# Performance work log

Hardware: AMD Instinct MI355X
Metric: run time of the kernel (lower is better)

The kernel has to match this reference:

```python
import jax, jax.numpy as jnp
import numpy as np

TOKENS, D_IN, D_OUT = 8192, 4096, 11008


def setup_inputs() -> dict:
    key = jax.random.key(0)
    k1, k2, k3, k4 = jax.random.split(key, 4)
    x = jax.random.normal(k1, (TOKENS, D_IN), dtype=jnp.float32)
    # int8-range quantized weight (stored int32; values in [-127, 127] simulated via [0,127])
    weight_q = jax.random.randint(k2, (D_OUT, D_IN), -127, 128, dtype=jnp.int32)
    # per-output-row scale (abs-max / 127), small positive values
    max_val = jax.random.uniform(k3, (D_OUT,), dtype=jnp.float32, minval=1e-3, maxval=0.02)
    bias = jax.random.normal(k4, (D_OUT,), dtype=jnp.float32)
    return {"x": x, "weight_q": weight_q, "max_val": max_val, "bias": bias}


def reference(x, weight_q, max_val, bias):
    # dequantize: w[o, i] = weight_q[o, i] * max_val[o]   (per-row scale)
    w = weight_q.astype(x.dtype) * max_val[:, None]          # [D_OUT, D_IN]
    # linear: y = x @ w.T + bias
    return jnp.einsum('ti,oi->to', x, w) + bias               # [TOKENS, D_OUT]
```

## Files before the change

### kernel.cpp

```cpp
#include <hip/hip_runtime.h>


#define M_TOK 8192
#define K_DIM 4096
#define N_OUT 11008
#define BM 256
#define BN 256
#define BK 64
#define NT (K_DIM / BK)
#define NBM (M_TOK / BM)
#define NBN (N_OUT / BN)
#define NWG (NBM * NBN)
#define SLOT 32768

typedef __attribute__((ext_vector_type(4))) int   i32x4;
typedef __attribute__((ext_vector_type(4))) float f32x4;
typedef __attribute__((ext_vector_type(4))) short bf16x4;
typedef __attribute__((ext_vector_type(8))) short bf16x8;
typedef unsigned short u16;
typedef signed char i8;
typedef unsigned char u8;

__global__ __launch_bounds__(256) void prep_fused(
    const float* __restrict__ x, i8* __restrict__ xq, float* __restrict__ sx,
    const int* __restrict__ win, i8* __restrict__ wout, long n16) {
  __shared__ float wmx[4];
  const int tid = threadIdx.x;
  if (blockIdx.x < M_TOK) {
    const int t = blockIdx.x;
    const float* row = x + (long)t * K_DIM;
    f32x4 v[4];
    float mx = 0.0f;
#pragma unroll
    for (int j = 0; j < 4; ++j) {
      v[j] = ((const f32x4*)row)[tid * 4 + j];
#pragma unroll
      for (int e = 0; e < 4; ++e) mx = fmaxf(mx, fabsf(v[j][e]));
    }
#pragma unroll
    for (int off = 32; off >= 1; off >>= 1) mx = fmaxf(mx, __shfl_xor(mx, off));
    if ((tid & 63) == 0) wmx[tid >> 6] = mx;
    __syncthreads();
    mx = fmaxf(fmaxf(wmx[0], wmx[1]), fmaxf(wmx[2], wmx[3]));
    const float sxinv = (mx > 0.0f) ? 127.0f / mx : 0.0f;
    if (tid == 0) sx[t] = (mx > 0.0f) ? mx / 127.0f : 0.0f;
    i32x4 out;
#pragma unroll
    for (int j = 0; j < 4; ++j) {
      int q0 = __float2int_rn(v[j][0] * sxinv);
      int q1 = __float2int_rn(v[j][1] * sxinv);
      int q2 = __float2int_rn(v[j][2] * sxinv);
      int q3 = __float2int_rn(v[j][3] * sxinv);
      q0 = max(-127, min(127, q0)); q1 = max(-127, min(127, q1));
      q2 = max(-127, min(127, q2)); q3 = max(-127, min(127, q3));
      out[j] = (q0 & 255) | ((q1 & 255) << 8) | ((q2 & 255) << 16) | ((q3 & 255) << 24);
    }
    ((i32x4*)(xq + (long)t * K_DIM))[tid] = out;
  } else {
    long i = (long)(blockIdx.x - M_TOK) * blockDim.x + tid;
    const long stride = 2048L * blockDim.x;
    for (; i < n16; i += stride) {
      i32x4 o;
#pragma unroll
      for (int j = 0; j < 4; ++j) {
        i32x4 w = ((const i32x4*)win)[i * 4 + j];
        o[j] = (w[0] & 255) | ((w[1] & 255) << 8) | ((w[2] & 255) << 16) | ((w[3] & 255) << 24);
      }
      ((i32x4*)wout)[i] = o;
    }
  }
}

__device__ __forceinline__ void gl_lds16(const i8* g, u8* l) {
  __builtin_amdgcn_global_load_lds(
      (const __attribute__((address_space(1))) void*)g,
      (__attribute__((address_space(3))) void*)l,
      16, 0, 0);
}

#define STAGE(T) do { \
    u8* wp = lds + ((T) & 3) * SLOT; \
    const int ko_ = (T) * BK; \
    gl_lds16(pA + ko_, wp + dwa); \
    gl_lds16(pB + ko_, wp + 16384 + dwa); \
  } while (0)

#define TILE(T, ST, CNTASM) do { \
    const char* pa_ = ldsc + ((T) & 3) * SLOT + abase; \
    const char* pb_ = ldsc + ((T) & 3) * SLOT + bbase; \
    i32x4 af[4], bv[4]; \
    _Pragma("unroll") \
    for (int m = 0; m < 4; ++m) af[m] = *(const i32x4*)(pa_ + m * 1024); \
    _Pragma("unroll") \
    for (int n = 0; n < 4; ++n) bv[n] = *(const i32x4*)(pb_ + n * 1024); \
    if (ST) STAGE((T) + 3); \
    __builtin_amdgcn_s_setprio(1); \
    _Pragma("unroll") \
    for (int m = 0; m < 4; ++m) \
      _Pragma("unroll") \
      for (int n = 0; n < 4; ++n) \
        acc[m][n] = __builtin_amdgcn_mfma_i32_16x16x64_i8(af[m], bv[n], acc[m][n], 0, 0, 0); \
    __builtin_amdgcn_s_setprio(0); \
    asm volatile(CNTASM ::: "memory"); \
    __builtin_amdgcn_sched_barrier(0); \
    __builtin_amdgcn_s_barrier(); \
  } while (0)

__global__ __launch_bounds__(1024, 4) void gemm_i8(
    const i8* __restrict__ A, const i8* __restrict__ B,
    const float* __restrict__ sx, const float* __restrict__ scale,
    const float* __restrict__ bias, float* __restrict__ C) {
  __shared__ u8 lds[4 * SLOT];

  const int tid  = threadIdx.x;
  const int lane = tid & 63;
  const int wave = tid >> 6;
  const int wm = wave >> 2;
  const int wn = wave & 3;

  const int swz = (blockIdx.x & 7) * (NWG / 8) + (blockIdx.x >> 3);
  const int bm = swz / NBN;
  const int bn = swz % NBN;
  const long m0 = (long)bm * BM;
  const long n0 = (long)bn * BN;

  const int rs = tid >> 2;
  const int cs = ((tid & 3) * 16) ^ (((tid >> 3) & 3) << 4);
  const i8* pA = A + (m0 + rs) * (long)K_DIM + cs;
  const i8* pB = B + (n0 + rs) * (long)K_DIM + cs;
  const int dwa = wave * 1024;

  const int inner = ((lane >> 4) * 16) ^ ((((lane & 15) >> 1) & 3) << 4);
  const int abase = (wm * 64 + (lane & 15)) * 64 + inner;
  const int bbase = 16384 + (wn * 64 + (lane & 15)) * 64 + inner;
  const char* ldsc = (const char*)lds;

  i32x4 acc[4][4] = {};

  STAGE(0); STAGE(1); STAGE(2);
  asm volatile("s_waitcnt vmcnt(4)" ::: "memory");
  __builtin_amdgcn_sched_barrier(0);
  __builtin_amdgcn_s_barrier();

  for (int t = 0; t < NT - 3; ++t) {
    TILE(t, 1, "s_waitcnt vmcnt(4)");
  }
  TILE(NT - 3, 0, "s_waitcnt vmcnt(2)");
  TILE(NT - 2, 0, "s_waitcnt vmcnt(0)");
  TILE(NT - 1, 0, "s_waitcnt vmcnt(0)");

  const int crow = (lane >> 4) * 4;
  const int ccol = lane & 15;
  float sxa[4][4];
#pragma unroll
  for (int m = 0; m < 4; ++m)
#pragma unroll
    for (int v = 0; v < 4; ++v)
      sxa[m][v] = sx[m0 + wm * 64 + m * 16 + crow + v];
#pragma unroll
  for (int n = 0; n < 4; ++n) {
    const long col = n0 + wn * 64 + n * 16 + ccol;
    const float sc = scale[col];
    const float bz = bias[col];
#pragma unroll
    for (int m = 0; m < 4; ++m) {
      const long row = m0 + wm * 64 + m * 16 + crow;
      i32x4 a = acc[m][n];
#pragma unroll
      for (int v = 0; v < 4; ++v)
        C[(row + v) * (long)N_OUT + col] = (float)a[v] * (sc * sxa[m][v]) + bz;
    }
  }
}

__device__ __forceinline__ u16 to_bf16_rne(float f) {
  union { float f; unsigned u; } v; v.f = f;
  return (u16)((v.u + 0x7FFFu + ((v.u >> 16) & 1u)) >> 16);
}

__global__ __launch_bounds__(256) void gemm_cvt(
    const float* __restrict__ X, const int* __restrict__ W,
    const float* __restrict__ scale, const float* __restrict__ bias,
    float* __restrict__ C) {
  __shared__ u16 lds_a[128 * 32];
  __shared__ u16 lds_b[128 * 32];

  const int tid  = threadIdx.x;
  const int lane = tid & 63;
  const int wave = tid >> 6;
  const int wm = wave >> 1, wn = wave & 1;

  const long m0 = (long)blockIdx.y * 128;
  const long n0 = (long)blockIdx.x * 128;

  const int arow = tid >> 3;
  const int acol = (tid & 7) * 4;

  const float* gX = X + (m0 + arow) * (long)K_DIM + acol;
  const int*   gW = W + (n0 + arow) * (long)K_DIM + acol;

  u16* wla = lds_a + arow * 32 + acol;
  u16* wlb = lds_b + arow * 32 + acol;

  f32x4 acc[4][4] = {};
  const int fr = lane & 15;
  const int fk = (lane >> 4) * 8;
  const u16* fa = lds_a + (wm * 64 + fr) * 32 + fk;
  const u16* fb = lds_b + (wn * 64 + fr) * 32 + fk;

  for (int kk = 0; kk < K_DIM / 32; ++kk) {
    const long ko = (long)kk * 32;
    f32x4 xv[4]; i32x4 wv[4];
#pragma unroll
    for (int j = 0; j < 4; ++j) {
      xv[j] = *(const f32x4*)(gX + (long)j * 32 * K_DIM + ko);
      wv[j] = *(const i32x4*)(gW + (long)j * 32 * K_DIM + ko);
    }
    __syncthreads();
#pragma unroll
    for (int j = 0; j < 4; ++j) {
      bf16x4 oa, ob;
      oa.x = (short)to_bf16_rne(xv[j][0]);
      oa.y = (short)to_bf16_rne(xv[j][1]);
      oa.z = (short)to_bf16_rne(xv[j][2]);
      oa.w = (short)to_bf16_rne(xv[j][3]);
      ob.x = (short)to_bf16_rne((float)wv[j][0]);
      ob.y = (short)to_bf16_rne((float)wv[j][1]);
      ob.z = (short)to_bf16_rne((float)wv[j][2]);
      ob.w = (short)to_bf16_rne((float)wv[j][3]);
      *(bf16x4*)(wla + j * 32 * 32) = oa;
      *(bf16x4*)(wlb + j * 32 * 32) = ob;
    }
    __syncthreads();

    bf16x8 af[4], bfr[4];
#pragma unroll
    for (int m = 0; m < 4; ++m) af[m] = *(const bf16x8*)(fa + m * 16 * 32);
#pragma unroll
    for (int n = 0; n < 4; ++n) bfr[n] = *(const bf16x8*)(fb + n * 16 * 32);
#pragma unroll
    for (int m = 0; m < 4; ++m)
#pragma unroll
      for (int n = 0; n < 4; ++n)
        acc[m][n] = __builtin_amdgcn_mfma_f32_16x16x32_bf16(af[m], bfr[n], acc[m][n], 0, 0, 0);
  }

  const int crow = (lane >> 4) * 4;
  const int ccol = lane & 15;
#pragma unroll
  for (int n = 0; n < 4; ++n) {
    const long col = n0 + wn * 64 + n * 16 + ccol;
    const float sc = scale[col];
    const float bz = bias[col];
#pragma unroll
    for (int m = 0; m < 4; ++m) {
      const long row = m0 + wm * 64 + m * 16 + crow;
      f32x4 a = acc[m][n];
#pragma unroll
      for (int v = 0; v < 4; ++v)
        C[(row + v) * (long)N_OUT + col] = a[v] * sc + bz;
    }
  }
}

extern "C" void kernel_launch(void* const* d_in, const int* in_sizes, int n_in,
                              void* d_out, int out_size, void* d_ws, size_t ws_size,
                              hipStream_t stream) {
  const float* x  = (const float*)d_in[0];
  const int*   wq = (const int*)d_in[1];
  const float* mx = (const float*)d_in[2];
  const float* bs = (const float*)d_in[3];
  float* out = (float*)d_out;

  const size_t szXQ = (size_t)M_TOK * K_DIM;
  const size_t szWQ = (size_t)N_OUT * K_DIM;
  const size_t szSX = (size_t)M_TOK * sizeof(float);
  if (ws_size >= szXQ + szWQ + szSX) {
    i8* xq = (i8*)d_ws;
    i8* wq8 = xq + szXQ;
    float* sx = (float*)(wq8 + szWQ);
    prep_fused<<<M_TOK + 2048, 256, 0, stream>>>(x, xq, sx, wq, wq8,
                                                 (long)N_OUT * K_DIM / 16);
    gemm_i8<<<dim3(NWG), dim3(1024), 0, stream>>>(xq, wq8, sx, mx, bs, out);
  } else {
    dim3 grid(N_OUT / 128, M_TOK / 128);
    gemm_cvt<<<grid, 256, 0, stream>>>(x, wq, mx, bs, out);
  }
}
```

Measured before the change: 477.7 us.

## Double-buffer A fragments in registers and prefetch next tile from LDS

A-operand fragments for tile T+1 are now read from LDS during tile T into alternating register sets (afE/afO), so those LDS reads overlap the current tile's MFMAs. The main loop is unrolled by two to alternate the buffers. The MFMA loop order is swapped to n-outer. The vmcnt waits are tightened from 4 to 2 so the next stage's global-to-LDS loads have landed one tile earlier, which shortens the effective prefetch distance and adds register pressure.

```diff
diff --git a/kernel.cpp b/kernel.cpp
--- a/kernel.cpp
+++ b/kernel.cpp
@@ -85,21 +85,23 @@
     gl_lds16(pB + ko_, wp + 16384 + dwa); \
   } while (0)
 
-#define TILE(T, ST, CNTASM) do { \
-    const char* pa_ = ldsc + ((T) & 3) * SLOT + abase; \
+#define TILE(T, AFC, AFN, RA, ST, CNTASM) do { \
     const char* pb_ = ldsc + ((T) & 3) * SLOT + bbase; \
-    i32x4 af[4], bv[4]; \
-    _Pragma("unroll") \
-    for (int m = 0; m < 4; ++m) af[m] = *(const i32x4*)(pa_ + m * 1024); \
+    i32x4 bv[4]; \
     _Pragma("unroll") \
     for (int n = 0; n < 4; ++n) bv[n] = *(const i32x4*)(pb_ + n * 1024); \
+    if (RA) { \
+      const char* pa1_ = ldsc + (((T) + 1) & 3) * SLOT + abase; \
+      _Pragma("unroll") \
+      for (int m = 0; m < 4; ++m) AFN[m] = *(const i32x4*)(pa1_ + m * 1024); \
+    } \
     if (ST) STAGE((T) + 3); \
     __builtin_amdgcn_s_setprio(1); \
     _Pragma("unroll") \
-    for (int m = 0; m < 4; ++m) \
+    for (int n = 0; n < 4; ++n) \
       _Pragma("unroll") \
-      for (int n = 0; n < 4; ++n) \
-        acc[m][n] = __builtin_amdgcn_mfma_i32_16x16x64_i8(af[m], bv[n], acc[m][n], 0, 0, 0); \
+      for (int m = 0; m < 4; ++m) \
+        acc[m][n] = __builtin_amdgcn_mfma_i32_16x16x64_i8(AFC[m], bv[n], acc[m][n], 0, 0, 0); \
     __builtin_amdgcn_s_setprio(0); \
     asm volatile(CNTASM ::: "memory"); \
     __builtin_amdgcn_sched_barrier(0); \
@@ -136,18 +138,26 @@
   const char* ldsc = (const char*)lds;
 
   i32x4 acc[4][4] = {};
+  i32x4 afE[4], afO[4];
 
   STAGE(0); STAGE(1); STAGE(2);
-  asm volatile("s_waitcnt vmcnt(4)" ::: "memory");
+  asm volatile("s_waitcnt vmcnt(2)" ::: "memory");
   __builtin_amdgcn_sched_barrier(0);
   __builtin_amdgcn_s_barrier();
-
-  for (int t = 0; t < NT - 3; ++t) {
-    TILE(t, 1, "s_waitcnt vmcnt(4)");
-  }
-  TILE(NT - 3, 0, "s_waitcnt vmcnt(2)");
-  TILE(NT - 2, 0, "s_waitcnt vmcnt(0)");
-  TILE(NT - 1, 0, "s_waitcnt vmcnt(0)");
+  {
+    const char* qa = ldsc + abase;
+#pragma unroll
+    for (int m = 0; m < 4; ++m) afE[m] = *(const i32x4*)(qa + m * 1024);
+  }
+
+  for (int t = 0; t < 60; t += 2) {
+    TILE(t,     afE, afO, 1, 1, "s_waitcnt vmcnt(2)");
+    TILE(t + 1, afO, afE, 1, 1, "s_waitcnt vmcnt(2)");
+  }
+  TILE(60, afE, afO, 1, 1, "s_waitcnt vmcnt(2)");
+  TILE(61, afO, afE, 1, 0, "s_waitcnt vmcnt(0)");
+  TILE(62, afE, afO, 1, 0, "s_waitcnt vmcnt(0)");
+  TILE(63, afO, afE, 0, 0, "s_waitcnt vmcnt(0)");
 
   const int crow = (lane >> 4) * 4;
   const int ccol = lane & 15;
```

After: 511.3 us. +7.0%, slower.

## Restructure int8 GEMM to 512 threads, BK=128, double-buffered sub-tile pipeline

Applied to the files above, without the earlier changes.

Halves the workgroup to 8 waves, each now computing a 128x64 output block with 8x4 accumulators, and doubles BK to 128. Each K-tile is split into two 64-wide halves, and each half is computed in two phases. Global-to-LDS loads for the next tile are interleaved between these phases, replacing the previous 4-slot ring. The aim is more MFMA work per LDS fragment load, since B fragments are reused across 8 M sub-tiles, and better overlap of loads with compute. In exchange it roughly doubles accumulator registers, adds more barriers per tile, and uses 128KB of LDS, which may limit occupancy.

```diff
diff --git a/kernel.cpp b/kernel.cpp
--- a/kernel.cpp
+++ b/kernel.cpp
@@ -6,12 +6,11 @@
 #define N_OUT 11008
 #define BM 256
 #define BN 256
-#define BK 64
+#define BK 128
 #define NT (K_DIM / BK)
 #define NBM (M_TOK / BM)
 #define NBN (N_OUT / BN)
 #define NWG (NBM * NBN)
-#define SLOT 32768
 
 typedef __attribute__((ext_vector_type(4))) int   i32x4;
 typedef __attribute__((ext_vector_type(4))) float f32x4;
@@ -78,22 +77,37 @@
       16, 0, 0);
 }
 
-#define STAGE(T) do { \
-    u8* wp = lds + ((T) & 3) * SLOT; \
-    const int ko_ = (T) * BK; \
-    gl_lds16(pA + ko_, wp + dwa); \
-    gl_lds16(pB + ko_, wp + 16384 + dwa); \
+#define SA(KT, SUB) do { \
+    const int bo_ = (((KT) & 1) << 16) + ((SUB) << 14); \
+    const i8* s_ = pA0 + (KT) * BK + (SUB) * 64; \
+    gl_lds16(s_, lds + bo_ + dwa); \
+    gl_lds16(s_ + 128L * K_DIM, lds + bo_ + 8192 + dwa); \
   } while (0)
-
-#define TILE(T, ST, CNTASM) do { \
-    const char* pa_ = ldsc + ((T) & 3) * SLOT + abase; \
-    const char* pb_ = ldsc + ((T) & 3) * SLOT + bbase; \
+#define SB(KT, SUB) do { \
+    const int bo_ = (((KT) & 1) << 16) + 32768 + ((SUB) << 14); \
+    const i8* s_ = pB0 + (KT) * BK + (SUB) * 64; \
+    gl_lds16(s_, lds + bo_ + dwa); \
+    gl_lds16(s_ + 128L * K_DIM, lds + bo_ + 8192 + dwa); \
+  } while (0)
+
+#define BAR() __builtin_amdgcn_s_barrier()
+#define LGKM0() do { asm volatile("s_waitcnt lgkmcnt(0)" ::: "memory"); \
+                     __builtin_amdgcn_sched_barrier(0); } while (0)
+
+#define TILE(T, S12, S34, C2, C4) do { \
+    const char* base_ = ldsc + (((T) & 1) << 16); \
+    const char* pa0_ = base_ + abase;             \
+    const char* pa1_ = base_ + 16384 + abase;     \
+    const char* pb0_ = base_ + 32768 + bbase;     \
+    const char* pb1_ = base_ + 49152 + bbase;     \
     i32x4 af[4], bv[4]; \
-    _Pragma("unroll") \
-    for (int m = 0; m < 4; ++m) af[m] = *(const i32x4*)(pa_ + m * 1024); \
-    _Pragma("unroll") \
-    for (int n = 0; n < 4; ++n) bv[n] = *(const i32x4*)(pb_ + n * 1024); \
-    if (ST) STAGE((T) + 3); \
+     \
+    _Pragma("unroll") \
+    for (int m = 0; m < 4; ++m) af[m] = *(const i32x4*)(pa0_ + m * 1024); \
+    _Pragma("unroll") \
+    for (int n = 0; n < 4; ++n) bv[n] = *(const i32x4*)(pb0_ + n * 1024); \
+    if (S12) SA((T) + 1, 1); \
+    BAR(); LGKM0(); \
     __builtin_amdgcn_s_setprio(1); \
     _Pragma("unroll") \
     for (int m = 0; m < 4; ++m) \
@@ -101,16 +115,62 @@
       for (int n = 0; n < 4; ++n) \
         acc[m][n] = __builtin_amdgcn_mfma_i32_16x16x64_i8(af[m], bv[n], acc[m][n], 0, 0, 0); \
     __builtin_amdgcn_s_setprio(0); \
-    asm volatile(CNTASM ::: "memory"); \
+    BAR(); \
+     \
+    i32x4 ag[4]; \
+    _Pragma("unroll") \
+    for (int m = 0; m < 4; ++m) ag[m] = *(const i32x4*)(pa0_ + (m + 4) * 1024); \
+    if (S12) SB((T) + 1, 1); \
+    BAR(); LGKM0(); \
+    __builtin_amdgcn_s_setprio(1); \
+    _Pragma("unroll") \
+    for (int m = 0; m < 4; ++m) \
+      _Pragma("unroll") \
+      for (int n = 0; n < 4; ++n) \
+        acc[m + 4][n] = __builtin_amdgcn_mfma_i32_16x16x64_i8(ag[m], bv[n], acc[m + 4][n], 0, 0, 0); \
+    __builtin_amdgcn_s_setprio(0); \
+    asm volatile(C2 ::: "memory"); \
     __builtin_amdgcn_sched_barrier(0); \
-    __builtin_amdgcn_s_barrier(); \
+    BAR(); \
+     \
+    i32x4 af1[4], bw[4]; \
+    _Pragma("unroll") \
+    for (int m = 0; m < 4; ++m) af1[m] = *(const i32x4*)(pa1_ + m * 1024); \
+    _Pragma("unroll") \
+    for (int n = 0; n < 4; ++n) bw[n] = *(const i32x4*)(pb1_ + n * 1024); \
+    if (S34) SA((T) + 2, 0); \
+    BAR(); LGKM0(); \
+    __builtin_amdgcn_s_setprio(1); \
+    _Pragma("unroll") \
+    for (int m = 0; m < 4; ++m) \
+      _Pragma("unroll") \
+      for (int n = 0; n < 4; ++n) \
+        acc[m][n] = __builtin_amdgcn_mfma_i32_16x16x64_i8(af1[m], bw[n], acc[m][n], 0, 0, 0); \
+    __builtin_amdgcn_s_setprio(0); \
+    BAR(); \
+     \
+    i32x4 ag1[4]; \
+    _Pragma("unroll") \
+    for (int m = 0; m < 4; ++m) ag1[m] = *(const i32x4*)(pa1_ + (m + 4) * 1024); \
+    if (S34) SB((T) + 2, 0); \
+    BAR(); LGKM0(); \
+    __builtin_amdgcn_s_setprio(1); \
+    _Pragma("unroll") \
+    for (int m = 0; m < 4; ++m) \
+      _Pragma("unroll") \
+      for (int n = 0; n < 4; ++n) \
+        acc[m + 4][n] = __builtin_amdgcn_mfma_i32_16x16x64_i8(ag1[m], bw[n], acc[m + 4][n], 0, 0, 0); \
+    __builtin_amdgcn_s_setprio(0); \
+    asm volatile(C4 ::: "memory"); \
+    __builtin_amdgcn_sched_barrier(0); \
+    BAR(); \
   } while (0)
 
-__global__ __launch_bounds__(1024, 4) void gemm_i8(
+__global__ __launch_bounds__(512, 2) void gemm_i8(
     const i8* __restrict__ A, const i8* __restrict__ B,
     const float* __restrict__ sx, const float* __restrict__ scale,
     const float* __restrict__ bias, float* __restrict__ C) {
-  __shared__ u8 lds[4 * SLOT];
+  __shared__ u8 lds[131072];
 
   const int tid  = threadIdx.x;
   const int lane = tid & 63;
@@ -126,45 +186,44 @@
 
   const int rs = tid >> 2;
   const int cs = ((tid & 3) * 16) ^ (((tid >> 3) & 3) << 4);
-  const i8* pA = A + (m0 + rs) * (long)K_DIM + cs;
-  const i8* pB = B + (n0 + rs) * (long)K_DIM + cs;
+  const i8* pA0 = A + (m0 + rs) * (long)K_DIM + cs;
+  const i8* pB0 = B + (n0 + rs) * (long)K_DIM + cs;
   const int dwa = wave * 1024;
 
   const int inner = ((lane >> 4) * 16) ^ ((((lane & 15) >> 1) & 3) << 4);
-  const int abase = (wm * 64 + (lane & 15)) * 64 + inner;
-  const int bbase = 16384 + (wn * 64 + (lane & 15)) * 64 + inner;
+  const int abase = (wm * 128 + (lane & 15)) * 64 + inner;
+  const int bbase = (wn * 64 + (lane & 15)) * 64 + inner;
   const char* ldsc = (const char*)lds;
 
-  i32x4 acc[4][4] = {};
-
-  STAGE(0); STAGE(1); STAGE(2);
+  i32x4 acc[8][4] = {};
+
+  SA(0, 0); SB(0, 0); SA(0, 1); SB(0, 1); SA(1, 0); SB(1, 0);
   asm volatile("s_waitcnt vmcnt(4)" ::: "memory");
   __builtin_amdgcn_sched_barrier(0);
-  __builtin_amdgcn_s_barrier();
-
-  for (int t = 0; t < NT - 3; ++t) {
-    TILE(t, 1, "s_waitcnt vmcnt(4)");
-  }
-  TILE(NT - 3, 0, "s_waitcnt vmcnt(2)");
-  TILE(NT - 2, 0, "s_waitcnt vmcnt(0)");
-  TILE(NT - 1, 0, "s_waitcnt vmcnt(0)");
+  BAR();
+
+  for (int t = 0; t < NT - 2; ++t) {
+    TILE(t, 1, 1, "s_waitcnt vmcnt(4)", "s_waitcnt vmcnt(4)");
+  }
+  TILE(NT - 2, 1, 0, "s_waitcnt vmcnt(4)", "s_waitcnt vmcnt(4)");
+  TILE(NT - 1, 0, 0, "s_waitcnt vmcnt(0)", "s_waitcnt vmcnt(0)");
 
   const int crow = (lane >> 4) * 4;
   const int ccol = lane & 15;
-  float sxa[4][4];
-#pragma unroll
-  for (int m = 0; m < 4; ++m)
+  float sxa[8][4];
+#pragma unroll
+  for (int m = 0; m < 8; ++m)
 #pragma unroll
     for (int v = 0; v < 4; ++v)
-      sxa[m][v] = sx[m0 + wm * 64 + m * 16 + crow + v];
+      sxa[m][v] = sx[m0 + wm * 128 + m * 16 + crow + v];
 #pragma unroll
   for (int n = 0; n < 4; ++n) {
     const long col = n0 + wn * 64 + n * 16 + ccol;
     const float sc = scale[col];
     const float bz = bias[col];
 #pragma unroll
-    for (int m = 0; m < 4; ++m) {
-      const long row = m0 + wm * 64 + m * 16 + crow;
+    for (int m = 0; m < 8; ++m) {
+      const long row = m0 + wm * 128 + m * 16 + crow;
       i32x4 a = acc[m][n];
 #pragma unroll
       for (int v = 0; v < 4; ++v)
@@ -281,7 +340,7 @@
     float* sx = (float*)(wq8 + szWQ);
     prep_fused<<<M_TOK + 2048, 256, 0, stream>>>(x, xq, sx, wq, wq8,
                                                  (long)N_OUT * K_DIM / 16);
-    gemm_i8<<<dim3(NWG), dim3(1024), 0, stream>>>(xq, wq8, sx, mx, bs, out);
+    gemm_i8<<<dim3(NWG), dim3(512), 0, stream>>>(xq, wq8, sx, mx, bs, out);
   } else {
     dim3 grid(N_OUT / 128, M_TOK / 128);
     gemm_cvt<<<grid, 256, 0, stream>>>(x, wq, mx, bs, out);
```

Result: slower. 498.9 us (+4.4%).

## Shrink GEMM tile to 256x128 with 512 threads and triple-buffered LDS

Applied to the files above, without the earlier changes.

Changes the int8 GEMM workgroup tile from 256x256 to 256x128 and runs 512 threads (8 waves in a 4x2 layout) instead of 1024. The LDS ring drops from four 32KB slots to three 24KB slots with prefetch distance 2, and the main loop is unrolled by three so slot offsets are compile-time constants. The aim is smaller LDS and thread footprints so more workgroups fit per CU and 11008 columns tile evenly, at the cost of less operand reuse per tile and a shallower prefetch pipeline.

```diff
diff --git a/kernel.cpp b/kernel.cpp
--- a/kernel.cpp
+++ b/kernel.cpp
@@ -5,13 +5,13 @@
 #define K_DIM 4096
 #define N_OUT 11008
 #define BM 256
-#define BN 256
+#define BN 128
 #define BK 64
 #define NT (K_DIM / BK)
 #define NBM (M_TOK / BM)
 #define NBN (N_OUT / BN)
 #define NWG (NBM * NBN)
-#define SLOT 32768
+#define SLOT 24576
 
 typedef __attribute__((ext_vector_type(4))) int   i32x4;
 typedef __attribute__((ext_vector_type(4))) float f32x4;
@@ -78,22 +78,22 @@
       16, 0, 0);
 }
 
-#define STAGE(T) do { \
-    u8* wp = lds + ((T) & 3) * SLOT; \
+#define STAGE(T, WS) do { \
+    u8* wp = lds + (WS); \
     const int ko_ = (T) * BK; \
-    gl_lds16(pA + ko_, wp + dwa); \
-    gl_lds16(pB + ko_, wp + 16384 + dwa); \
+    gl_lds16(pA0 + ko_, wp + dwa); \
+    gl_lds16(pA1 + ko_, wp + 8192 + dwa); \
+    gl_lds16(pB0 + ko_, wp + 16384 + dwa); \
   } while (0)
 
-#define TILE(T, ST, CNTASM) do { \
-    const char* pa_ = ldsc + ((T) & 3) * SLOT + abase; \
-    const char* pb_ = ldsc + ((T) & 3) * SLOT + bbase; \
+#define TCOMP(RS) do { \
+    const char* pa_ = ldsc + (RS) + abase; \
+    const char* pb_ = ldsc + (RS) + bbase; \
     i32x4 af[4], bv[4]; \
     _Pragma("unroll") \
     for (int m = 0; m < 4; ++m) af[m] = *(const i32x4*)(pa_ + m * 1024); \
     _Pragma("unroll") \
     for (int n = 0; n < 4; ++n) bv[n] = *(const i32x4*)(pb_ + n * 1024); \
-    if (ST) STAGE((T) + 3); \
     __builtin_amdgcn_s_setprio(1); \
     _Pragma("unroll") \
     for (int m = 0; m < 4; ++m) \
@@ -101,22 +101,27 @@
       for (int n = 0; n < 4; ++n) \
         acc[m][n] = __builtin_amdgcn_mfma_i32_16x16x64_i8(af[m], bv[n], acc[m][n], 0, 0, 0); \
     __builtin_amdgcn_s_setprio(0); \
+  } while (0)
+
+#define TILE(RS, WS, T, ST, CNTASM) do { \
+    if (ST) STAGE((T) + 2, WS); \
+    TCOMP(RS); \
     asm volatile(CNTASM ::: "memory"); \
     __builtin_amdgcn_sched_barrier(0); \
     __builtin_amdgcn_s_barrier(); \
   } while (0)
 
-__global__ __launch_bounds__(1024, 4) void gemm_i8(
+__global__ __launch_bounds__(512, 4) void gemm_i8(
     const i8* __restrict__ A, const i8* __restrict__ B,
     const float* __restrict__ sx, const float* __restrict__ scale,
     const float* __restrict__ bias, float* __restrict__ C) {
-  __shared__ u8 lds[4 * SLOT];
+  __shared__ u8 lds[3 * SLOT];
 
   const int tid  = threadIdx.x;
   const int lane = tid & 63;
   const int wave = tid >> 6;
-  const int wm = wave >> 2;
-  const int wn = wave & 3;
+  const int wm = wave >> 1;
+  const int wn = wave & 1;
 
   const int swz = (blockIdx.x & 7) * (NWG / 8) + (blockIdx.x >> 3);
   const int bm = swz / NBN;
@@ -126,8 +131,9 @@
 
   const int rs = tid >> 2;
   const int cs = ((tid & 3) * 16) ^ (((tid >> 3) & 3) << 4);
-  const i8* pA = A + (m0 + rs) * (long)K_DIM + cs;
-  const i8* pB = B + (n0 + rs) * (long)K_DIM + cs;
+  const i8* pA0 = A + (m0 + rs) * (long)K_DIM + cs;
+  const i8* pA1 = pA0 + 128L * K_DIM;
+  const i8* pB0 = B + (n0 + rs) * (long)K_DIM + cs;
   const int dwa = wave * 1024;
 
   const int inner = ((lane >> 4) * 16) ^ ((((lane & 15) >> 1) & 3) << 4);
@@ -137,17 +143,22 @@
 
   i32x4 acc[4][4] = {};
 
-  STAGE(0); STAGE(1); STAGE(2);
-  asm volatile("s_waitcnt vmcnt(4)" ::: "memory");
+  STAGE(0, 0);
+  STAGE(1, SLOT);
+  asm volatile("s_waitcnt vmcnt(3)" ::: "memory");
   __builtin_amdgcn_sched_barrier(0);
   __builtin_amdgcn_s_barrier();
 
-  for (int t = 0; t < NT - 3; ++t) {
-    TILE(t, 1, "s_waitcnt vmcnt(4)");
-  }
-  TILE(NT - 3, 0, "s_waitcnt vmcnt(2)");
-  TILE(NT - 2, 0, "s_waitcnt vmcnt(0)");
-  TILE(NT - 1, 0, "s_waitcnt vmcnt(0)");
+  for (int tt = 0; tt < 20; ++tt) {
+    const int t = tt * 3;
+    TILE(0 * SLOT, 2 * SLOT, t,     1, "s_waitcnt vmcnt(3)");
+    TILE(1 * SLOT, 0 * SLOT, t + 1, 1, "s_waitcnt vmcnt(3)");
+    TILE(2 * SLOT, 1 * SLOT, t + 2, 1, "s_waitcnt vmcnt(3)");
+  }
+  TILE(0 * SLOT, 2 * SLOT, 60, 1, "s_waitcnt vmcnt(3)");
+  TILE(1 * SLOT, 0 * SLOT, 61, 1, "s_waitcnt vmcnt(3)");
+  TILE(2 * SLOT, 0,        62, 0, "s_waitcnt vmcnt(0)");
+  TILE(0 * SLOT, 0,        63, 0, "s_waitcnt vmcnt(0)");
 
   const int crow = (lane >> 4) * 4;
   const int ccol = lane & 15;
@@ -281,7 +292,7 @@
     float* sx = (float*)(wq8 + szWQ);
     prep_fused<<<M_TOK + 2048, 256, 0, stream>>>(x, xq, sx, wq, wq8,
                                                  (long)N_OUT * K_DIM / 16);
-    gemm_i8<<<dim3(NWG), dim3(1024), 0, stream>>>(xq, wq8, sx, mx, bs, out);
+    gemm_i8<<<dim3(NWG), dim3(512), 0, stream>>>(xq, wq8, sx, mx, bs, out);
   } else {
     dim3 grid(N_OUT / 128, M_TOK / 128);
     gemm_cvt<<<grid, 256, 0, stream>>>(x, wq, mx, bs, out);
```

After: 490.2 us. 1.03x slower.
